# Kernel tuning notes

Hardware: AMD Instinct MI355X
Metric: run time of the kernel (lower is better)

## Reference

```python
import jax, jax.numpy as jnp
import numpy as np

N = 100000
IN_DIM = 1280
HID = 128
EPS = 1e-5

def _gconv(x, src, dst, W, b, n):
    # DGL GraphConv, norm='both': D_out^{-1/2} gather -> sum -> D_in^{-1/2}, then W, b.
    # Project first (in_feats >= out_feats here) so edge messages are HID-dim.
    ones = jnp.ones(src.shape[0], dtype=x.dtype)
    out_deg = jnp.clip(jax.ops.segment_sum(ones, src, num_segments=n), 1.0)
    in_deg = jnp.clip(jax.ops.segment_sum(ones, dst, num_segments=n), 1.0)
    h = (x * (out_deg ** -0.5)[:, None]) @ W          # [n, HID]
    agg = jax.ops.segment_sum(h[src], dst, num_segments=n)  # scatter-add over edges
    return agg * (in_deg ** -0.5)[:, None] + b

def _batchnorm(x, g, b):
    m = x.mean(0)
    v = jnp.mean((x - m) ** 2, axis=0)  # biased variance (torch BN normalization)
    return (x - m) * jax.lax.rsqrt(v + EPS) * g + b

def _layer(x, edges, W, b, fcW, fcb, g, beta, n):
    # HeteroGraphConv aggregate='sum' over 3 relations, then FC + ReLU + BN
    h = _gconv(x, edges[0][0], edges[0][1], W[0], b[0], n)
    h = h + _gconv(x, edges[1][0], edges[1][1], W[1], b[1], n)
    h = h + _gconv(x, edges[2][0], edges[2][1], W[2], b[2], n)
    h = h @ fcW + fcb
    h = jax.nn.relu(h)
    return _batchnorm(h, g, beta)

def setup_inputs() -> dict:
    key = jax.random.key(0)
    ks = jax.random.split(key, 16)
    x = jax.random.normal(ks[0], (N, IN_DIM), dtype=jnp.float32)
    seq_edges = jax.random.randint(ks[1], (2, 200000), 0, N, dtype=jnp.int32)
    knn_edges = jax.random.randint(ks[2], (2, 1000000), 0, N, dtype=jnp.int32)
    dis_edges = jax.random.randint(ks[3], (2, 1600000), 0, N, dtype=jnp.int32)
    s_in = 1.0 / np.sqrt(IN_DIM)
    s_h = 1.0 / np.sqrt(HID)
    W0 = jax.random.normal(ks[4], (3, IN_DIM, HID), dtype=jnp.float32) * s_in
    b0 = jnp.zeros((3, HID), dtype=jnp.float32)
    fcW0 = jax.random.normal(ks[5], (HID, HID), dtype=jnp.float32) * s_h
    fcb0 = jnp.zeros((HID,), dtype=jnp.float32)
    g0 = jnp.ones((HID,), dtype=jnp.float32)
    beta0 = jnp.zeros((HID,), dtype=jnp.float32)
    W1 = jax.random.normal(ks[6], (3, HID, HID), dtype=jnp.float32) * s_h
    b1 = jnp.zeros((3, HID), dtype=jnp.float32)
    fcW1 = jax.random.normal(ks[7], (HID, HID), dtype=jnp.float32) * s_h
    fcb1 = jnp.zeros((HID,), dtype=jnp.float32)
    g1 = jnp.ones((HID,), dtype=jnp.float32)
    beta1 = jnp.zeros((HID,), dtype=jnp.float32)
    return {"x": x, "seq_edges": seq_edges, "knn_edges": knn_edges, "dis_edges": dis_edges,
            "W0": W0, "b0": b0, "fcW0": fcW0, "fcb0": fcb0, "g0": g0, "beta0": beta0,
            "W1": W1, "b1": b1, "fcW1": fcW1, "fcb1": fcb1, "g1": g1, "beta1": beta1}

def reference(x, seq_edges, knn_edges, dis_edges,
              W0, b0, fcW0, fcb0, g0, beta0,
              W1, b1, fcW1, fcb1, g1, beta1):
    edges = [seq_edges, knn_edges, dis_edges]
    n = x.shape[0]
    h = _layer(x, edges, W0, b0, fcW0, fcb0, g0, beta0, n)
    # dropout after non-final layers is identity at eval
    h = _layer(h, edges, W1, b1, fcW1, fcb1, g1, beta1, n)
    return h
```

## Files before the change

kernel.cpp:

```cpp
#include <hip/hip_runtime.h>
#include <hip/hip_bf16.h>
#include <math.h>

#define NN 100000
#define HID 128
#define EPSV 1e-5f

typedef short bf16x8 __attribute__((ext_vector_type(8)));
typedef float f32x4 __attribute__((ext_vector_type(4)));
typedef unsigned short u16;

__device__ __forceinline__ u16 f2b(float f) {
  unsigned u = __builtin_bit_cast(unsigned, f);
  u += 0x7FFFu + ((u >> 16) & 1u);
  return (u16)(u >> 16);
}
__device__ __forceinline__ float b2f(u16 h) {
  unsigned u = ((unsigned)h) << 16;
  return __builtin_bit_cast(float, u);
}

#define AS1(p) ((__attribute__((address_space(1))) void*)(p))
#define AS3(p) ((__attribute__((address_space(3))) void*)(p))


static __global__ void k_zero(float* __restrict__ p, int n) {
  int i = blockIdx.x * blockDim.x + threadIdx.x;
  if (i < n) p[i] = 0.f;
}

static __global__ void k_zero_i(int* __restrict__ p, int n) {
  int i = blockIdx.x * blockDim.x + threadIdx.x;
  if (i < n) p[i] = 0;
}

static __global__ void k_deg(const int* __restrict__ src, const int* __restrict__ dst,
                             int E, float* __restrict__ outdeg, float* __restrict__ indeg) {
  int e = blockIdx.x * blockDim.x + threadIdx.x;
  if (e < E) {
    atomicAdd(&outdeg[src[e]], 1.f);
    atomicAdd(&indeg[dst[e]], 1.f);
  }
}

static __global__ void k_counts(const float* __restrict__ indegRaw, int* __restrict__ counts, int n3) {
  int i = blockIdx.x * blockDim.x + threadIdx.x;
  if (i < n3) counts[i] = (int)indegRaw[i];
  else if (i == n3) counts[i] = 0;
}

static __global__ void k_rsqrt_clip(float* __restrict__ p, int n) {
  int i = blockIdx.x * blockDim.x + threadIdx.x;
  if (i < n) p[i] = rsqrtf(fmaxf(p[i], 1.f));
}

static __global__ void k_scan1(const int* __restrict__ in, int* __restrict__ out,
                               int* __restrict__ aux, int n) {
  __shared__ int s[256];
  int t = threadIdx.x, i = blockIdx.x * 256 + t;
  int v = (i < n) ? in[i] : 0;
  s[t] = v; __syncthreads();
#pragma unroll
  for (int d = 1; d < 256; d <<= 1) {
    int x = (t >= d) ? s[t - d] : 0;
    __syncthreads();
    s[t] += x;
    __syncthreads();
  }
  if (i < n) out[i] = s[t] - v;
  if (t == 255) aux[blockIdx.x] = s[255];
}

static __global__ void k_scan2(int* __restrict__ aux, int nb) {
  __shared__ int s[256];
  __shared__ int carry;
  int t = threadIdx.x;
  if (t == 0) carry = 0;
  __syncthreads();
  for (int base = 0; base < nb; base += 256) {
    int i = base + t;
    int v = (i < nb) ? aux[i] : 0;
    s[t] = v; __syncthreads();
#pragma unroll
    for (int d = 1; d < 256; d <<= 1) {
      int x = (t >= d) ? s[t - d] : 0;
      __syncthreads();
      s[t] += x;
      __syncthreads();
    }
    int excl = s[t] - v + carry;
    if (i < nb) aux[i] = excl;
    int tot = s[255];
    __syncthreads();
    if (t == 0) carry += tot;
    __syncthreads();
  }
}

static __global__ void k_scan3(int* __restrict__ out, const int* __restrict__ aux, int n) {
  int i = blockIdx.x * 256 + threadIdx.x;
  if (i < n) out[i] += aux[blockIdx.x];
}

static __global__ void k_fill(const int* __restrict__ src, const int* __restrict__ dst, int E,
                              const int* __restrict__ off, int* __restrict__ cur,
                              int rbase, int* __restrict__ srt) {
  int e = blockIdx.x * blockDim.x + threadIdx.x;
  if (e < E) {
    int d = dst[e];
    int p = off[rbase + d] + atomicAdd(&cur[rbase + d], 1);
    srt[p] = src[e];
  }
}

static __global__ void k_cvt_w(const float* __restrict__ W, u16* __restrict__ Wt, int K) {
  int i = blockIdx.x * blockDim.x + threadIdx.x;
  int tot = 3 * K * 128;
  if (i < tot) {
    int rel = i / (K * 128);
    int rem = i - rel * K * 128;
    int k = rem >> 7;
    int c = rem & 127;
    Wt[((size_t)rel * 128 + c) * K + k] = f2b(W[i]);
  }
}

static __global__ void k_cvt_fcw(const float* __restrict__ W, u16* __restrict__ Bt) {
  int i = blockIdx.x * blockDim.x + threadIdx.x;
  if (i < 128 * 128) {
    int k = i >> 7, c = i & 127;
    Bt[c * 128 + k] = f2b(W[i]);
  }
}

template<int K, bool AF32>
__global__ __launch_bounds__(512)
void k_gemm_pipe(const void* __restrict__ Av,
                 const u16* __restrict__ Wt,
                 const float* __restrict__ sout,
                 u16* __restrict__ Y,
                 int M)
{
  constexpr int A_BYTES = AF32 ? (128 * 32 * 4) : (128 * 32 * 2);
  constexpr int B_BYTES = 384 * 32 * 2;
  constexpr int BUF_U16 = (A_BYTES + B_BYTES) / 2;
  __shared__ u16 lds[3][BUF_U16];

  const int row0 = blockIdx.x * 128;
  const int t    = threadIdx.x;
  const int lane = t & 63;
  const int w    = t >> 6;
  const int wm   = w >> 2;
  const int wn   = w & 3;
  const int l15  = lane & 15, l4 = lane >> 4;
  const int kl   = l4 * 8;
  const int nk   = K / 32;

  int ar = row0 + w * 16 + l15;  if (ar >= M) ar = M - 1;

  const float* Af = (const float*)Av;
  const u16*   Ab = (const u16*)Av;

  const u16* gb0 = Wt + (size_t)(w * 48 +      l15) * K + kl;
  const u16* gb1 = Wt + (size_t)(w * 48 + 16 + l15) * K + kl;
  const u16* gb2 = Wt + (size_t)(w * 48 + 32 + l15) * K + kl;

  auto STAGE = [&](int buf, int k0) {
    u16* L = &lds[buf][0];
    if constexpr (AF32) {
      const float* sa = Af + (size_t)ar * K + k0 + l4 * 8;
      __builtin_amdgcn_global_load_lds(AS1(sa),     AS3(L + (w * 2048) / 2),          16, 0, 0);
      __builtin_amdgcn_global_load_lds(AS1(sa + 4), AS3(L + (w * 2048 + 1024) / 2),   16, 0, 0);
    } else {
      const u16* sa = Ab + (size_t)ar * K + k0 + kl;
      __builtin_amdgcn_global_load_lds(AS1(sa),     AS3(L + (w * 1024) / 2),          16, 0, 0);
    }
    u16* Bd = L + A_BYTES / 2;
    __builtin_amdgcn_global_load_lds(AS1(gb0 + k0), AS3(Bd + (w * 3 + 0) * 512), 16, 0, 0);
    __builtin_amdgcn_global_load_lds(AS1(gb1 + k0), AS3(Bd + (w * 3 + 1) * 512), 16, 0, 0);
    __builtin_amdgcn_global_load_lds(AS1(gb2 + k0), AS3(Bd + (w * 3 + 2) * 512), 16, 0, 0);
  };

  f32x4 acc[4][6];
#pragma unroll
  for (int m = 0; m < 4; ++m)
#pragma unroll
    for (int n = 0; n < 6; ++n) acc[m][n] = (f32x4){0.f, 0.f, 0.f, 0.f};

  STAGE(0, 0);
  if (nk > 1) STAGE(1, 32);

  for (int k = 0; k < nk; ++k) {
    if (k + 1 < nk) {
      if constexpr (AF32) asm volatile("s_waitcnt vmcnt(5)" ::: "memory");
      else                asm volatile("s_waitcnt vmcnt(4)" ::: "memory");
    } else {
      asm volatile("s_waitcnt vmcnt(0)" ::: "memory");
    }
    __builtin_amdgcn_sched_barrier(0);
    __builtin_amdgcn_s_barrier();
    __builtin_amdgcn_sched_barrier(0);

    if (k + 2 < nk) STAGE((k + 2) % 3, (k + 2) * 32);

    const int cur = k % 3;
    bf16x8 a[4], b[6];
    if constexpr (AF32) {
      const float* Al = (const float*)&lds[cur][0];
#pragma unroll
      for (int m = 0; m < 4; ++m) {
        f32x4 lo = *(const f32x4*)&Al[(wm * 4 + m) * 512 + lane * 4];
        f32x4 hi = *(const f32x4*)&Al[(wm * 4 + m) * 512 + 256 + lane * 4];
        union { bf16x8 v; u16 u[8]; } q;
#pragma unroll
        for (int j = 0; j < 4; ++j) {
          q.u[j]     = __builtin_bit_cast(u16, __float2bfloat16(lo[j]));
          q.u[4 + j] = __builtin_bit_cast(u16, __float2bfloat16(hi[j]));
        }
        a[m] = q.v;
      }
    } else {
      const u16* Al = &lds[cur][0];
#pragma unroll
      for (int m = 0; m < 4; ++m) a[m] = *(const bf16x8*)&Al[(wm * 4 + m) * 512 + lane * 8];
    }
    {
      const u16* Bl = &lds[cur][A_BYTES / 2];
#pragma unroll
      for (int n = 0; n < 6; ++n) b[n] = *(const bf16x8*)&Bl[(wn * 6 + n) * 512 + lane * 8];
    }

    __builtin_amdgcn_s_setprio(1);
#pragma unroll
    for (int m = 0; m < 4; ++m)
#pragma unroll
      for (int n = 0; n < 6; ++n)
        acc[m][n] = __builtin_amdgcn_mfma_f32_16x16x32_bf16(a[m], b[n], acc[m][n], 0, 0, 0);
    __builtin_amdgcn_s_setprio(0);
  }

#pragma unroll
  for (int m = 0; m < 4; ++m) {
    const int rb = row0 + wm * 64 + m * 16 + l4 * 4;
#pragma unroll
    for (int j = 0; j < 4; ++j) {
      const int row = rb + j;
      if (row < M) {
        u16* yrow = Y + (size_t)row * 384;
#pragma unroll
        for (int n = 0; n < 6; ++n) {
          const int c = wn * 96 + n * 16;
          const float sc = sout[(size_t)(c >> 7) * NN + row];
          yrow[c + l15] = f2b(acc[m][n][j] * sc);
        }
      }
    }
  }
}

static __global__ __launch_bounds__(256)
void k_gather(const int* __restrict__ off, const int* __restrict__ srt,
              const float* __restrict__ sin_, const u16* __restrict__ Y,
              const float* __restrict__ b, u16* __restrict__ acc16)
{
  int d = blockIdx.x * 4 + (threadIdx.x >> 6);
  if (d >= NN) return;
  int c = (threadIdx.x & 63) * 2;
  float v0 = b[c]     + b[128 + c]     + b[256 + c];
  float v1 = b[c + 1] + b[128 + c + 1] + b[256 + c + 1];
#pragma unroll
  for (int r = 0; r < 3; ++r) {
    int base = r * NN + d;
    int j0 = off[base], j1 = off[base + 1];
    float p0 = 0.f, p1 = 0.f;
    int j = j0;
    for (; j + 4 <= j1; j += 4) {
      int s0 = srt[j], s1 = srt[j + 1], s2 = srt[j + 2], s3 = srt[j + 3];
      unsigned u0 = *(const unsigned*)&Y[(size_t)s0 * 384 + r * 128 + c];
      unsigned u1 = *(const unsigned*)&Y[(size_t)s1 * 384 + r * 128 + c];
      unsigned u2 = *(const unsigned*)&Y[(size_t)s2 * 384 + r * 128 + c];
      unsigned u3 = *(const unsigned*)&Y[(size_t)s3 * 384 + r * 128 + c];
      p0 += b2f((u16)(u0 & 0xFFFFu)) + b2f((u16)(u1 & 0xFFFFu))
          + b2f((u16)(u2 & 0xFFFFu)) + b2f((u16)(u3 & 0xFFFFu));
      p1 += b2f((u16)(u0 >> 16)) + b2f((u16)(u1 >> 16))
          + b2f((u16)(u2 >> 16)) + b2f((u16)(u3 >> 16));
    }
    for (; j < j1; ++j) {
      int s = srt[j];
      unsigned u = *(const unsigned*)&Y[(size_t)s * 384 + r * 128 + c];
      p0 += b2f((u16)(u & 0xFFFFu));
      p1 += b2f((u16)(u >> 16));
    }
    float sc = sin_[base];
    v0 += p0 * sc;
    v1 += p1 * sc;
  }
  unsigned out = (unsigned)f2b(v0) | ((unsigned)f2b(v1) << 16);
  *(unsigned*)&acc16[(size_t)d * 128 + c] = out;
}

static __global__ __launch_bounds__(512)
void k_fc_mfma(const u16* __restrict__ A,
               const u16* __restrict__ Bt,
               const float* __restrict__ bias,
               float* __restrict__ Z, int M)
{
  __shared__ u16 Ab[4][4096];

  const int row0 = blockIdx.x * 128;
  const int t    = threadIdx.x;
  const int lane = t & 63;
  const int w    = t >> 6;
  const int wm   = w >> 2;
  const int wn   = w & 3;
  const int l15  = lane & 15, l4 = lane >> 4;
  const int kl   = l4 * 8;

  int ar = row0 + w * 16 + l15;  if (ar >= M) ar = M - 1;

  bf16x8 br[2][4];
#pragma unroll
  for (int n = 0; n < 2; ++n)
#pragma unroll
    for (int ks = 0; ks < 4; ++ks)
      br[n][ks] = *(const bf16x8*)&Bt[(size_t)(wn * 32 + n * 16 + l15) * 128 + ks * 32 + kl];

#pragma unroll
  for (int ks = 0; ks < 4; ++ks)
    __builtin_amdgcn_global_load_lds(AS1(A + (size_t)ar * 128 + ks * 32 + kl),
                                     AS3(&Ab[ks][w * 512]), 16, 0, 0);

  asm volatile("s_waitcnt vmcnt(0)" ::: "memory");
  __syncthreads();

  f32x4 acc[4][2];
#pragma unroll
  for (int m = 0; m < 4; ++m) { acc[m][0] = (f32x4){0,0,0,0}; acc[m][1] = (f32x4){0,0,0,0}; }

#pragma unroll
  for (int ks = 0; ks < 4; ++ks) {
#pragma unroll
    for (int m = 0; m < 4; ++m) {
      bf16x8 a = *(const bf16x8*)&Ab[ks][(wm * 4 + m) * 512 + lane * 8];
      acc[m][0] = __builtin_amdgcn_mfma_f32_16x16x32_bf16(a, br[0][ks], acc[m][0], 0, 0, 0);
      acc[m][1] = __builtin_amdgcn_mfma_f32_16x16x32_bf16(a, br[1][ks], acc[m][1], 0, 0, 0);
    }
  }

#pragma unroll
  for (int m = 0; m < 4; ++m) {
    const int rb = row0 + wm * 64 + m * 16 + l4 * 4;
#pragma unroll
    for (int j = 0; j < 4; ++j) {
      const int row = rb + j;
      if (row < M) {
#pragma unroll
        for (int n = 0; n < 2; ++n) {
          const int cc = wn * 32 + n * 16 + l15;
          Z[(size_t)row * 128 + cc] = fmaxf(acc[m][n][j] + bias[cc], 0.f);
        }
      }
    }
  }
}

static __global__ void k_bn_stats(const float* __restrict__ Z, int M, float* __restrict__ stats) {
  int col = threadIdx.x;
  float s = 0.f, s2 = 0.f;
  for (int row = blockIdx.x; row < M; row += gridDim.x) {
    float v = Z[(size_t)row * 128 + col];
    s += v;
    s2 += v * v;
  }
  atomicAdd(&stats[col], s);
  atomicAdd(&stats[128 + col], s2);
}

static __global__ void k_bn_finalize(const float* __restrict__ stats, int M,
                                     const float* __restrict__ g, const float* __restrict__ beta,
                                     float* __restrict__ ab) {
  int j = threadIdx.x;
  float m  = stats[j] / (float)M;
  float v  = stats[128 + j] / (float)M - m * m;
  float inv = rsqrtf(v + EPSV) * g[j];
  ab[j]       = inv;
  ab[128 + j] = beta[j] - m * inv;
}

template<bool OUT_BF16>
static __global__ void k_bn_apply(const float* __restrict__ Z, const float* __restrict__ ab,
                                  void* __restrict__ out, int n) {
  int i = blockIdx.x * blockDim.x + threadIdx.x;
  if (i < n) {
    int j = i & 127;
    float v = Z[i] * ab[j] + ab[128 + j];
    if constexpr (OUT_BF16) ((u16*)out)[i] = f2b(v);
    else                    ((float*)out)[i] = v;
  }
}


template<int K, bool AF32, bool OUT_BF16>
static void run_layer(const void* X,
                      const u16* Wt, const float* b,
                      const u16* fcWt, const float* fcb,
                      const float* g, const float* beta,
                      const int* off, const int* srt,
                      float* sOut, float* sIn, u16* Y, float* Z, u16* acc16,
                      float* stats, float* ab, void* out, hipStream_t stream)
{
  const int NT = (NN + 127) / 128;
  k_gemm_pipe<K, AF32><<<NT, 512, 0, stream>>>(X, Wt, sOut, Y, NN);

  k_gather<<<(NN + 3) / 4, 256, 0, stream>>>(off, srt, sIn, Y, b, acc16);

  k_fc_mfma<<<NT, 512, 0, stream>>>(acc16, fcWt, fcb, Z, NN);

  k_zero<<<1, 256, 0, stream>>>(stats, 256);
  k_bn_stats<<<1024, 128, 0, stream>>>(Z, NN, stats);
  k_bn_finalize<<<1, 128, 0, stream>>>(stats, NN, g, beta, ab);
  k_bn_apply<OUT_BF16><<<(NN * HID + 255) / 256, 256, 0, stream>>>(Z, ab, out, NN * HID);
}

extern "C" void kernel_launch(void* const* d_in, const int* in_sizes, int n_in,
                              void* d_out, int out_size, void* d_ws, size_t ws_size,
                              hipStream_t stream)
{
  const float* x    = (const float*)d_in[0];
  const int*   seq  = (const int*)d_in[1];
  const int*   knn  = (const int*)d_in[2];
  const int*   dis  = (const int*)d_in[3];
  const float* W0   = (const float*)d_in[4];
  const float* b0   = (const float*)d_in[5];
  const float* fcW0 = (const float*)d_in[6];
  const float* fcb0 = (const float*)d_in[7];
  const float* g0   = (const float*)d_in[8];
  const float* be0  = (const float*)d_in[9];
  const float* W1   = (const float*)d_in[10];
  const float* b1   = (const float*)d_in[11];
  const float* fcW1 = (const float*)d_in[12];
  const float* fcb1 = (const float*)d_in[13];
  const float* g1   = (const float*)d_in[14];
  const float* be1  = (const float*)d_in[15];

  const int E[3] = { in_sizes[1] / 2, in_sizes[2] / 2, in_sizes[3] / 2 };
  const int* srcs[3] = { seq, knn, dis };

  const size_t N = NN;
  const int M3 = 3 * NN;

  float* ws    = (float*)d_ws;
  float* sOut  = ws;
  float* sIn   = sOut + 3 * N;
  u16*   acc16 = (u16*)(sIn + 3 * N);
  float* accF  = (float*)acc16;
  float* stats = accF + N * 128;
  float* ab    = stats + 256;
  u16*   Y     = (u16*)(ab + 256);
  float* Z     = (float*)Y;
  u16*   h16   = Y + N * 384;
  u16*   Wt0   = h16 + N * 128;
  u16*   Wt1   = Wt0 + 3 * 128 * 1280;
  u16*   fcWt0 = Wt1 + 3 * 128 * 128;
  u16*   fcWt1 = fcWt0 + 128 * 128;
  int*   counts= (int*)(fcWt1 + 128 * 128);
  int*   off   = counts + (M3 + 1);
  int*   aux   = off + (M3 + 1);
  int*   cur   = aux + 1536;
  int*   srt   = cur + M3;

  k_cvt_w<<<(3 * 1280 * 128 + 255) / 256, 256, 0, stream>>>(W0, Wt0, 1280);
  k_cvt_w<<<(3 * 128 * 128 + 255) / 256, 256, 0, stream>>>(W1, Wt1, 128);
  k_cvt_fcw<<<(128 * 128 + 255) / 256, 256, 0, stream>>>(fcW0, fcWt0);
  k_cvt_fcw<<<(128 * 128 + 255) / 256, 256, 0, stream>>>(fcW1, fcWt1);

  k_zero<<<(6 * NN + 255) / 256, 256, 0, stream>>>(sOut, 6 * NN);
  for (int r = 0; r < 3; ++r) {
    k_deg<<<(E[r] + 255) / 256, 256, 0, stream>>>(
        srcs[r], srcs[r] + E[r], E[r], sOut + (size_t)r * N, sIn + (size_t)r * N);
  }
  k_counts<<<(M3 + 1 + 255) / 256, 256, 0, stream>>>(sIn, counts, M3);
  k_rsqrt_clip<<<(6 * NN + 255) / 256, 256, 0, stream>>>(sOut, 6 * NN);

  const int nsc = M3 + 1;
  const int nb  = (nsc + 255) / 256;
  k_scan1<<<nb, 256, 0, stream>>>(counts, off, aux, nsc);
  k_scan2<<<1, 256, 0, stream>>>(aux, nb);
  k_scan3<<<nb, 256, 0, stream>>>(off, aux, nsc);

  k_zero_i<<<(M3 + 255) / 256, 256, 0, stream>>>(cur, M3);
  for (int r = 0; r < 3; ++r) {
    k_fill<<<(E[r] + 255) / 256, 256, 0, stream>>>(
        srcs[r], srcs[r] + E[r], E[r], off, cur, r * NN, srt);
  }

  run_layer<1280, true, true>(x, Wt0, b0, fcWt0, fcb0, g0, be0, off, srt,
                              sOut, sIn, Y, Z, acc16, stats, ab, h16, stream);

  run_layer<128, false, false>(h16, Wt1, b1, fcWt1, fcb1, g1, be1, off, srt,
                               sOut, sIn, Y, Z, acc16, stats, ab, d_out, stream);
}
```

Before: 1.299 ms.

## Split projection GEMM per relation with XCD-aware block mapping and double buffering

Replaces the 128x384-output, 512-thread, triple-buffered GEMM with a 128x128-per-relation kernel using 256 threads and double buffering. Block IDs are mapped so the three relation blocks for a row tile land on the same XCD, letting the shared A tile hit in L2. The intent is higher occupancy (launch bounds 3 blocks per SM), smaller LDS, and better L2 reuse. The risk is that the A operand is now read three times, and the shallower pipeline waits on vmcnt(0) each step.

```diff
diff --git a/kernel.cpp b/kernel.cpp
--- a/kernel.cpp
+++ b/kernel.cpp
@@ -134,77 +134,82 @@
 }
 
 template<int K, bool AF32>
-__global__ __launch_bounds__(512)
-void k_gemm_pipe(const void* __restrict__ Av,
-                 const u16* __restrict__ Wt,
-                 const float* __restrict__ sout,
-                 u16* __restrict__ Y,
-                 int M)
+__global__ __launch_bounds__(256, 3)
+void k_gemm2p(const void* __restrict__ Av,
+              const u16* __restrict__ Wt,
+              const float* __restrict__ sout,
+              u16* __restrict__ Y,
+              int M, int NT)
 {
-  constexpr int A_BYTES = AF32 ? (128 * 32 * 4) : (128 * 32 * 2);
-  constexpr int B_BYTES = 384 * 32 * 2;
-  constexpr int BUF_U16 = (A_BYTES + B_BYTES) / 2;
-  __shared__ u16 lds[3][BUF_U16];
-
-  const int row0 = blockIdx.x * 128;
+  constexpr int A_U16 = AF32 ? 8192 : 4096;
+  constexpr int B_U16 = 4096;
+  __shared__ u16 lds[2][A_U16 + B_U16];
+
+  const int bid  = blockIdx.x;
+  const int xcd  = bid & 7;
+  const int s    = bid >> 3;
+  const int rel  = s % 3;
+  const int tile = xcd + 8 * (s / 3);
+  if (tile >= NT) return;
+  const int row0 = tile * 128;
+
   const int t    = threadIdx.x;
   const int lane = t & 63;
   const int w    = t >> 6;
-  const int wm   = w >> 2;
-  const int wn   = w & 3;
+  const int wm   = w >> 1, wn = w & 1;
   const int l15  = lane & 15, l4 = lane >> 4;
   const int kl   = l4 * 8;
   const int nk   = K / 32;
 
-  int ar = row0 + w * 16 + l15;  if (ar >= M) ar = M - 1;
+  const u16* Wr = Wt + (size_t)rel * 128 * K;
+
+  int r0 = row0 + (2 * w) * 16 + l15;      if (r0 >= M) r0 = M - 1;
+  int r1 = row0 + (2 * w + 1) * 16 + l15;  if (r1 >= M) r1 = M - 1;
+
+  const u16* gb0 = Wr + (size_t)((2 * w) * 16 + l15) * K + kl;
+  const u16* gb1 = Wr + (size_t)((2 * w + 1) * 16 + l15) * K + kl;
 
   const float* Af = (const float*)Av;
   const u16*   Ab = (const u16*)Av;
-
-  const u16* gb0 = Wt + (size_t)(w * 48 +      l15) * K + kl;
-  const u16* gb1 = Wt + (size_t)(w * 48 + 16 + l15) * K + kl;
-  const u16* gb2 = Wt + (size_t)(w * 48 + 32 + l15) * K + kl;
 
   auto STAGE = [&](int buf, int k0) {
     u16* L = &lds[buf][0];
     if constexpr (AF32) {
-      const float* sa = Af + (size_t)ar * K + k0 + l4 * 8;
-      __builtin_amdgcn_global_load_lds(AS1(sa),     AS3(L + (w * 2048) / 2),          16, 0, 0);
-      __builtin_amdgcn_global_load_lds(AS1(sa + 4), AS3(L + (w * 2048 + 1024) / 2),   16, 0, 0);
+      const float* sa0 = Af + (size_t)r0 * K + k0 + kl;
+      const float* sa1 = Af + (size_t)r1 * K + k0 + kl;
+      __builtin_amdgcn_global_load_lds(AS1(sa0),     AS3(L + (2 * w) * 1024),       16, 0, 0);
+      __builtin_amdgcn_global_load_lds(AS1(sa0 + 4), AS3(L + (2 * w) * 1024 + 512), 16, 0, 0);
+      __builtin_amdgcn_global_load_lds(AS1(sa1),     AS3(L + (2 * w + 1) * 1024),       16, 0, 0);
+      __builtin_amdgcn_global_load_lds(AS1(sa1 + 4), AS3(L + (2 * w + 1) * 1024 + 512), 16, 0, 0);
     } else {
-      const u16* sa = Ab + (size_t)ar * K + k0 + kl;
-      __builtin_amdgcn_global_load_lds(AS1(sa),     AS3(L + (w * 1024) / 2),          16, 0, 0);
-    }
-    u16* Bd = L + A_BYTES / 2;
-    __builtin_amdgcn_global_load_lds(AS1(gb0 + k0), AS3(Bd + (w * 3 + 0) * 512), 16, 0, 0);
-    __builtin_amdgcn_global_load_lds(AS1(gb1 + k0), AS3(Bd + (w * 3 + 1) * 512), 16, 0, 0);
-    __builtin_amdgcn_global_load_lds(AS1(gb2 + k0), AS3(Bd + (w * 3 + 2) * 512), 16, 0, 0);
+      const u16* sa0 = Ab + (size_t)r0 * K + k0 + kl;
+      const u16* sa1 = Ab + (size_t)r1 * K + k0 + kl;
+      __builtin_amdgcn_global_load_lds(AS1(sa0), AS3(L + (2 * w) * 512),     16, 0, 0);
+      __builtin_amdgcn_global_load_lds(AS1(sa1), AS3(L + (2 * w + 1) * 512), 16, 0, 0);
+    }
+    u16* Bd = L + A_U16;
+    __builtin_amdgcn_global_load_lds(AS1(gb0 + k0), AS3(Bd + (2 * w) * 512),     16, 0, 0);
+    __builtin_amdgcn_global_load_lds(AS1(gb1 + k0), AS3(Bd + (2 * w + 1) * 512), 16, 0, 0);
   };
 
-  f32x4 acc[4][6];
+  f32x4 acc[4][4];
 #pragma unroll
   for (int m = 0; m < 4; ++m)
 #pragma unroll
-    for (int n = 0; n < 6; ++n) acc[m][n] = (f32x4){0.f, 0.f, 0.f, 0.f};
+    for (int n = 0; n < 4; ++n) acc[m][n] = (f32x4){0.f, 0.f, 0.f, 0.f};
 
   STAGE(0, 0);
-  if (nk > 1) STAGE(1, 32);
 
   for (int k = 0; k < nk; ++k) {
-    if (k + 1 < nk) {
-      if constexpr (AF32) asm volatile("s_waitcnt vmcnt(5)" ::: "memory");
-      else                asm volatile("s_waitcnt vmcnt(4)" ::: "memory");
-    } else {
-      asm volatile("s_waitcnt vmcnt(0)" ::: "memory");
-    }
+    asm volatile("s_waitcnt vmcnt(0)" ::: "memory");
     __builtin_amdgcn_sched_barrier(0);
     __builtin_amdgcn_s_barrier();
     __builtin_amdgcn_sched_barrier(0);
 
-    if (k + 2 < nk) STAGE((k + 2) % 3, (k + 2) * 32);
-
-    const int cur = k % 3;
-    bf16x8 a[4], b[6];
+    if (k + 1 < nk) STAGE((k + 1) & 1, (k + 1) * 32);
+
+    const int cur = k & 1;
+    bf16x8 a[4], b[4];
     if constexpr (AF32) {
       const float* Al = (const float*)&lds[cur][0];
 #pragma unroll
@@ -225,18 +230,16 @@
       for (int m = 0; m < 4; ++m) a[m] = *(const bf16x8*)&Al[(wm * 4 + m) * 512 + lane * 8];
     }
     {
-      const u16* Bl = &lds[cur][A_BYTES / 2];
-#pragma unroll
-      for (int n = 0; n < 6; ++n) b[n] = *(const bf16x8*)&Bl[(wn * 6 + n) * 512 + lane * 8];
-    }
-
-    __builtin_amdgcn_s_setprio(1);
+      const u16* Bl = &lds[cur][A_U16];
+#pragma unroll
+      for (int n = 0; n < 4; ++n) b[n] = *(const bf16x8*)&Bl[(wn * 4 + n) * 512 + lane * 8];
+    }
+
 #pragma unroll
     for (int m = 0; m < 4; ++m)
 #pragma unroll
-      for (int n = 0; n < 6; ++n)
+      for (int n = 0; n < 4; ++n)
         acc[m][n] = __builtin_amdgcn_mfma_f32_16x16x32_bf16(a[m], b[n], acc[m][n], 0, 0, 0);
-    __builtin_amdgcn_s_setprio(0);
   }
 
 #pragma unroll
@@ -246,13 +249,10 @@
     for (int j = 0; j < 4; ++j) {
       const int row = rb + j;
       if (row < M) {
-        u16* yrow = Y + (size_t)row * 384;
-#pragma unroll
-        for (int n = 0; n < 6; ++n) {
-          const int c = wn * 96 + n * 16;
-          const float sc = sout[(size_t)(c >> 7) * NN + row];
-          yrow[c + l15] = f2b(acc[m][n][j] * sc);
-        }
+        const float sc = sout[(size_t)rel * NN + row];
+        u16* yp = Y + (size_t)row * 384 + rel * 128 + wn * 64 + l15;
+#pragma unroll
+        for (int n = 0; n < 4; ++n) yp[n * 16] = f2b(acc[m][n][j] * sc);
       }
     }
   }
@@ -410,7 +410,8 @@
                       float* stats, float* ab, void* out, hipStream_t stream)
 {
   const int NT = (NN + 127) / 128;
-  k_gemm_pipe<K, AF32><<<NT, 512, 0, stream>>>(X, Wt, sOut, Y, NN);
+  const int nblk = 24 * ((NT + 7) / 8);
+  k_gemm2p<K, AF32><<<nblk, 256, 0, stream>>>(X, Wt, sOut, Y, NN, NT);
 
   k_gather<<<(NN + 3) / 4, 256, 0, stream>>>(off, srt, sIn, Y, b, acc16);
 
```

Result: slower. 1.360 ms (+4.8%).

## Merge per-relation CSR into one tagged CSR and fuse BN stats into FC

Applied to the files above, without the earlier changes.

Builds a single CSR over destination nodes for all three relations, packing the relation id into the low two bits of each source index. The gather kernel can then walk one combined edge list with an 8-wide unrolled loop that applies the per-relation in-degree scale per edge, instead of running three separate short loops. Batch-norm column sums and sums of squares are now accumulated inside the FC MFMA epilogue using shuffles, shared-memory atomics and then global atomics, which removes the separate pass that re-read Z. It also drops the s_setprio hints around the GEMM MFMA loop, and per-edge relation selection adds some ALU work in the gather.

```diff
diff --git a/kernel.cpp b/kernel.cpp
--- a/kernel.cpp
+++ b/kernel.cpp
@@ -43,10 +43,10 @@
   }
 }
 
-static __global__ void k_counts(const float* __restrict__ indegRaw, int* __restrict__ counts, int n3) {
-  int i = blockIdx.x * blockDim.x + threadIdx.x;
-  if (i < n3) counts[i] = (int)indegRaw[i];
-  else if (i == n3) counts[i] = 0;
+static __global__ void k_counts_tot(const float* __restrict__ indegRaw, int* __restrict__ counts, int n) {
+  int i = blockIdx.x * blockDim.x + threadIdx.x;
+  if (i < n) counts[i] = (int)(indegRaw[i] + indegRaw[n + i] + indegRaw[2 * n + i]);
+  else if (i == n) counts[i] = 0;
 }
 
 static __global__ void k_rsqrt_clip(float* __restrict__ p, int n) {
@@ -104,12 +104,12 @@
 
 static __global__ void k_fill(const int* __restrict__ src, const int* __restrict__ dst, int E,
                               const int* __restrict__ off, int* __restrict__ cur,
-                              int rbase, int* __restrict__ srt) {
+                              int rel, int* __restrict__ srt) {
   int e = blockIdx.x * blockDim.x + threadIdx.x;
   if (e < E) {
     int d = dst[e];
-    int p = off[rbase + d] + atomicAdd(&cur[rbase + d], 1);
-    srt[p] = src[e];
+    int p = off[d] + atomicAdd(&cur[d], 1);
+    srt[p] = (src[e] << 2) | rel;
   }
 }
 
@@ -230,13 +230,11 @@
       for (int n = 0; n < 6; ++n) b[n] = *(const bf16x8*)&Bl[(wn * 6 + n) * 512 + lane * 8];
     }
 
-    __builtin_amdgcn_s_setprio(1);
 #pragma unroll
     for (int m = 0; m < 4; ++m)
 #pragma unroll
       for (int n = 0; n < 6; ++n)
         acc[m][n] = __builtin_amdgcn_mfma_f32_16x16x32_bf16(a[m], b[n], acc[m][n], 0, 0, 0);
-    __builtin_amdgcn_s_setprio(0);
   }
 
 #pragma unroll
@@ -268,44 +266,45 @@
   int c = (threadIdx.x & 63) * 2;
   float v0 = b[c]     + b[128 + c]     + b[256 + c];
   float v1 = b[c + 1] + b[128 + c + 1] + b[256 + c + 1];
-#pragma unroll
-  for (int r = 0; r < 3; ++r) {
-    int base = r * NN + d;
-    int j0 = off[base], j1 = off[base + 1];
-    float p0 = 0.f, p1 = 0.f;
-    int j = j0;
-    for (; j + 4 <= j1; j += 4) {
-      int s0 = srt[j], s1 = srt[j + 1], s2 = srt[j + 2], s3 = srt[j + 3];
-      unsigned u0 = *(const unsigned*)&Y[(size_t)s0 * 384 + r * 128 + c];
-      unsigned u1 = *(const unsigned*)&Y[(size_t)s1 * 384 + r * 128 + c];
-      unsigned u2 = *(const unsigned*)&Y[(size_t)s2 * 384 + r * 128 + c];
-      unsigned u3 = *(const unsigned*)&Y[(size_t)s3 * 384 + r * 128 + c];
-      p0 += b2f((u16)(u0 & 0xFFFFu)) + b2f((u16)(u1 & 0xFFFFu))
-          + b2f((u16)(u2 & 0xFFFFu)) + b2f((u16)(u3 & 0xFFFFu));
-      p1 += b2f((u16)(u0 >> 16)) + b2f((u16)(u1 >> 16))
-          + b2f((u16)(u2 >> 16)) + b2f((u16)(u3 >> 16));
-    }
-    for (; j < j1; ++j) {
-      int s = srt[j];
-      unsigned u = *(const unsigned*)&Y[(size_t)s * 384 + r * 128 + c];
-      p0 += b2f((u16)(u & 0xFFFFu));
-      p1 += b2f((u16)(u >> 16));
-    }
-    float sc = sin_[base];
-    v0 += p0 * sc;
-    v1 += p1 * sc;
-  }
-  unsigned out = (unsigned)f2b(v0) | ((unsigned)f2b(v1) << 16);
-  *(unsigned*)&acc16[(size_t)d * 128 + c] = out;
+  const float sc0 = sin_[d], sc1 = sin_[NN + d], sc2 = sin_[2 * NN + d];
+  int j0 = off[d], j1 = off[d + 1];
+  int j = j0;
+  for (; j + 8 <= j1; j += 8) {
+    unsigned uu[8];
+    int rr[8];
+#pragma unroll
+    for (int q = 0; q < 8; ++q) {
+      int tg = srt[j + q];
+      rr[q] = tg & 3;
+      uu[q] = *(const unsigned*)&Y[(size_t)(tg >> 2) * 384 + (size_t)rr[q] * 128 + c];
+    }
+#pragma unroll
+    for (int q = 0; q < 8; ++q) {
+      float s = (rr[q] == 0) ? sc0 : ((rr[q] == 1) ? sc1 : sc2);
+      v0 = fmaf(b2f((u16)(uu[q] & 0xFFFFu)), s, v0);
+      v1 = fmaf(b2f((u16)(uu[q] >> 16)), s, v1);
+    }
+  }
+  for (; j < j1; ++j) {
+    int tg = srt[j];
+    int r = tg & 3;
+    unsigned u = *(const unsigned*)&Y[(size_t)(tg >> 2) * 384 + (size_t)r * 128 + c];
+    float s = (r == 0) ? sc0 : ((r == 1) ? sc1 : sc2);
+    v0 = fmaf(b2f((u16)(u & 0xFFFFu)), s, v0);
+    v1 = fmaf(b2f((u16)(u >> 16)), s, v1);
+  }
+  unsigned o = (unsigned)f2b(v0) | ((unsigned)f2b(v1) << 16);
+  *(unsigned*)&acc16[(size_t)d * 128 + c] = o;
 }
 
 static __global__ __launch_bounds__(512)
 void k_fc_mfma(const u16* __restrict__ A,
                const u16* __restrict__ Bt,
                const float* __restrict__ bias,
-               float* __restrict__ Z, int M)
+               float* __restrict__ Z, float* __restrict__ stats, int M)
 {
   __shared__ u16 Ab[4][4096];
+  __shared__ float sst[256];
 
   const int row0 = blockIdx.x * 128;
   const int t    = threadIdx.x;
@@ -316,6 +315,8 @@
   const int l15  = lane & 15, l4 = lane >> 4;
   const int kl   = l4 * 8;
 
+  if (t < 256) sst[t] = 0.f;
+
   int ar = row0 + w * 16 + l15;  if (ar >= M) ar = M - 1;
 
   bf16x8 br[2][4];
@@ -347,33 +348,39 @@
     }
   }
 
+  float ps[2] = {0.f, 0.f}, ps2[2] = {0.f, 0.f};
 #pragma unroll
   for (int m = 0; m < 4; ++m) {
     const int rb = row0 + wm * 64 + m * 16 + l4 * 4;
 #pragma unroll
     for (int j = 0; j < 4; ++j) {
       const int row = rb + j;
-      if (row < M) {
-#pragma unroll
-        for (int n = 0; n < 2; ++n) {
-          const int cc = wn * 32 + n * 16 + l15;
-          Z[(size_t)row * 128 + cc] = fmaxf(acc[m][n][j] + bias[cc], 0.f);
-        }
+      const bool ok = row < M;
+#pragma unroll
+      for (int n = 0; n < 2; ++n) {
+        const int cc = wn * 32 + n * 16 + l15;
+        float v = ok ? fmaxf(acc[m][n][j] + bias[cc], 0.f) : 0.f;
+        if (ok) Z[(size_t)row * 128 + cc] = v;
+        ps[n]  += v;
+        ps2[n] += v * v;
       }
     }
   }
-}
-
-static __global__ void k_bn_stats(const float* __restrict__ Z, int M, float* __restrict__ stats) {
-  int col = threadIdx.x;
-  float s = 0.f, s2 = 0.f;
-  for (int row = blockIdx.x; row < M; row += gridDim.x) {
-    float v = Z[(size_t)row * 128 + col];
-    s += v;
-    s2 += v * v;
-  }
-  atomicAdd(&stats[col], s);
-  atomicAdd(&stats[128 + col], s2);
+#pragma unroll
+  for (int n = 0; n < 2; ++n) {
+    ps[n]  += __shfl_xor(ps[n], 16);  ps[n]  += __shfl_xor(ps[n], 32);
+    ps2[n] += __shfl_xor(ps2[n], 16); ps2[n] += __shfl_xor(ps2[n], 32);
+  }
+  if (l4 == 0) {
+#pragma unroll
+    for (int n = 0; n < 2; ++n) {
+      const int cc = wn * 32 + n * 16 + l15;
+      atomicAdd(&sst[cc], ps[n]);
+      atomicAdd(&sst[128 + cc], ps2[n]);
+    }
+  }
+  __syncthreads();
+  if (t < 256) atomicAdd(&stats[t], sst[t]);
 }
 
 static __global__ void k_bn_finalize(const float* __restrict__ stats, int M,
@@ -410,14 +417,15 @@
                       float* stats, float* ab, void* out, hipStream_t stream)
 {
   const int NT = (NN + 127) / 128;
+
+  k_zero<<<1, 256, 0, stream>>>(stats, 256);
+
   k_gemm_pipe<K, AF32><<<NT, 512, 0, stream>>>(X, Wt, sOut, Y, NN);
 
   k_gather<<<(NN + 3) / 4, 256, 0, stream>>>(off, srt, sIn, Y, b, acc16);
 
-  k_fc_mfma<<<NT, 512, 0, stream>>>(acc16, fcWt, fcb, Z, NN);
-
-  k_zero<<<1, 256, 0, stream>>>(stats, 256);
-  k_bn_stats<<<1024, 128, 0, stream>>>(Z, NN, stats);
+  k_fc_mfma<<<NT, 512, 0, stream>>>(acc16, fcWt, fcb, Z, stats, NN);
+
   k_bn_finalize<<<1, 128, 0, stream>>>(stats, NN, g, beta, ab);
   k_bn_apply<OUT_BF16><<<(NN * HID + 255) / 256, 256, 0, stream>>>(Z, ab, out, NN * HID);
 }
@@ -447,7 +455,6 @@
   const int* srcs[3] = { seq, knn, dis };
 
   const size_t N = NN;
-  const int M3 = 3 * NN;
 
   float* ws    = (float*)d_ws;
   float* sOut  = ws;
@@ -464,10 +471,10 @@
   u16*   fcWt0 = Wt1 + 3 * 128 * 128;
   u16*   fcWt1 = fcWt0 + 128 * 128;
   int*   counts= (int*)(fcWt1 + 128 * 128);
-  int*   off   = counts + (M3 + 1);
-  int*   aux   = off + (M3 + 1);
+  int*   off   = counts + (NN + 1);
+  int*   aux   = off + (NN + 1);
   int*   cur   = aux + 1536;
-  int*   srt   = cur + M3;
+  int*   srt   = cur + NN;
 
   k_cvt_w<<<(3 * 1280 * 128 + 255) / 256, 256, 0, stream>>>(W0, Wt0, 1280);
   k_cvt_w<<<(3 * 128 * 128 + 255) / 256, 256, 0, stream>>>(W1, Wt1, 128);
@@ -479,19 +486,19 @@
     k_deg<<<(E[r] + 255) / 256, 256, 0, stream>>>(
         srcs[r], srcs[r] + E[r], E[r], sOut + (size_t)r * N, sIn + (size_t)r * N);
   }
-  k_counts<<<(M3 + 1 + 255) / 256, 256, 0, stream>>>(sIn, counts, M3);
+  k_counts_tot<<<(NN + 1 + 255) / 256, 256, 0, stream>>>(sIn, counts, NN);
   k_rsqrt_clip<<<(6 * NN + 255) / 256, 256, 0, stream>>>(sOut, 6 * NN);
 
-  const int nsc = M3 + 1;
+  const int nsc = NN + 1;
   const int nb  = (nsc + 255) / 256;
   k_scan1<<<nb, 256, 0, stream>>>(counts, off, aux, nsc);
   k_scan2<<<1, 256, 0, stream>>>(aux, nb);
   k_scan3<<<nb, 256, 0, stream>>>(off, aux, nsc);
 
-  k_zero_i<<<(M3 + 255) / 256, 256, 0, stream>>>(cur, M3);
+  k_zero_i<<<(NN + 255) / 256, 256, 0, stream>>>(cur, NN);
   for (int r = 0; r < 3; ++r) {
     k_fill<<<(E[r] + 255) / 256, 256, 0, stream>>>(
-        srcs[r], srcs[r] + E[r], E[r], off, cur, r * NN, srt);
+        srcs[r], srcs[r] + E[r], E[r], off, cur, r, srt);
   }
 
   run_layer<1280, true, true>(x, Wt0, b0, fcWt0, fcb0, g0, be0, off, srt,
```

Result: faster. 1.121 ms (-13.7%).
